# Kernel tuning notes

Hardware: AMD Instinct MI355X
Metric: run time of the kernel (lower is better)

Reference implementation:

```python
import jax, jax.numpy as jnp
from jax import lax
import numpy as np

B, ENC, H, DE, T = 16384, 512, 256, 32, 64


def setup_inputs() -> dict:
    key = jax.random.key(0)
    ks = jax.random.split(key, 12)
    s = lambda fan: 1.0 / np.sqrt(fan)
    return {
        "encoded_input_series": jax.random.normal(ks[0], (B, ENC), jnp.float32),
        "final_x_val": jax.random.normal(ks[1], (B, 1), jnp.float32),
        # embed_func: Dense(DE) applied to scalar input (last dim = 1)
        "W_emb": jax.random.normal(ks[2], (1, DE), jnp.float32) * s(1),
        "b_emb": jnp.zeros((DE,), jnp.float32),
        # encode_reshape layer: Dense(H) on encoded series -> initial h
        "W_enc": jax.random.normal(ks[3], (ENC, H), jnp.float32) * s(ENC),
        "b_enc": jnp.zeros((H,), jnp.float32),
        # LSTM cell params (Keras gate order i, f, c, o)
        "W_k": jax.random.normal(ks[4], (DE, 4 * H), jnp.float32) * s(DE),
        "W_r": jax.random.normal(ks[5], (H, 4 * H), jnp.float32) * s(H),
        "b_lstm": jnp.concatenate([jnp.zeros((H,)), jnp.ones((H,)), jnp.zeros((2 * H,))]).astype(jnp.float32),
        # reduce layer: Dense(1)
        "W_red": jax.random.normal(ks[6], (H, 1), jnp.float32) * s(H),
        "b_red": jnp.zeros((1,), jnp.float32),
        "decode_length": T,
    }


def reference(encoded_input_series, final_x_val, W_emb, b_emb, W_enc, b_enc,
              W_k, W_r, b_lstm, W_red, b_red, decode_length):
    Hdim = W_r.shape[0]
    # initial hidden state from encoder summary; cell state zero-initialized
    h0 = encoded_input_series @ W_enc + b_enc            # [B, H]
    c0 = jnp.zeros_like(h0)
    # initial decoder input: embed of last observed value
    x0 = final_x_val @ W_emb + b_emb                     # [B, DE]

    def step(carry, _):
        h, c, x = carry
        gates = x @ W_k + h @ W_r + b_lstm               # [B, 4H]
        i, f, cb, o = jnp.split(gates, 4, axis=-1)
        c_new = jax.nn.sigmoid(f) * c + jax.nn.sigmoid(i) * jnp.tanh(cb)
        h_new = jax.nn.sigmoid(o) * jnp.tanh(c_new)
        y = h_new @ W_red + b_red                        # [B, 1]
        x_next = y @ W_emb + b_emb
        return (h_new, c_new, x_next), y[:, 0]

    _, ys = lax.scan(step, (h0, c0, x0), None, length=decode_length)
    return ys.T                                          # [B, T]
```

## Files before the change

### kernel.cpp

```cpp
#include <hip/hip_runtime.h>
#include <hip/hip_bf16.h>
#include <math.h>


typedef _Float16 f16x8 __attribute__((ext_vector_type(8)));
typedef float f32x4 __attribute__((ext_vector_type(4)));

#define DEV __device__ __forceinline__

constexpr int ENC = 512;
constexpr int HD  = 256;
constexpr int DE  = 32;
constexpr int TT  = 64;
constexpr int NG  = 4 * HD;
constexpr int NKT = 8;
constexpr int TS  = 528;
constexpr int BR  = 64;
constexpr int NMT = 4;
constexpr int NW  = 16;
constexpr int WRS = 36;

constexpr float L2E = 1.44269504088896f;

DEV bool is_f32(const void* blstm) {
  return ((const unsigned*)blstm)[256] == 0x3F800000u;
}
DEV float ldf(const void* p, size_t i, bool f32) {
  return f32 ? ((const float*)p)[i]
             : __bfloat162float(((const __hip_bfloat16*)p)[i]);
}
DEV float gscale(int n) {
  return ((n >> 8) == 2) ? (2.0f * L2E) : L2E;
}
DEV void split2h(float v, _Float16& hi, _Float16& lo) {
  hi = (_Float16)v;
  lo = (_Float16)(v - (float)hi);
}
DEV void ld8cvt2h(const void* p, size_t i, bool f32, f16x8& hi, f16x8& lo) {
  if (f32) {
    const f32x4* q = (const f32x4*)((const float*)p + i);
    f32x4 u0 = q[0], u1 = q[1];
#pragma unroll
    for (int j = 0; j < 4; ++j) {
      float a = u0[j], b = u1[j];
      _Float16 ah = (_Float16)a, bh = (_Float16)b;
      hi[j] = ah; hi[4 + j] = bh;
      lo[j] = (_Float16)(a - (float)ah); lo[4 + j] = (_Float16)(b - (float)bh);
    }
  } else {
    const __hip_bfloat16* s = (const __hip_bfloat16*)p + i;
#pragma unroll
    for (int j = 0; j < 8; ++j) {
      float a = __bfloat162float(s[j]);
      _Float16 ah = (_Float16)a;
      hi[j] = ah;
      lo[j] = (_Float16)(a - (float)ah);
    }
  }
}
DEV f16x8 load8h(const _Float16* p) {
  return *reinterpret_cast<const f16x8*>(p);
}

DEV void waitflag(volatile int* f, int v) {
  while (*f < v) { __builtin_amdgcn_s_sleep(1); }
  asm volatile("" ::: "memory");
}
DEV void signalflag(volatile int* f, int v, int lane) {
  asm volatile("s_waitcnt lgkmcnt(0)" ::: "memory");
  if (lane == 0) *f = v;
}

__global__ __launch_bounds__(256) void pack_vec(const void* __restrict__ wemb,
                                                const void* __restrict__ bemb,
                                                const void* __restrict__ wk,
                                                const void* __restrict__ bl,
                                                const void* __restrict__ bredp,
                                                float* __restrict__ wk2n,
                                                float* __restrict__ wk2P,
                                                float* __restrict__ bp0P,
                                                float* __restrict__ bp2P) {
  const bool f32 = is_f32(bl);
  int n = blockIdx.x * 256 + threadIdx.x;
  if (n >= NG) return;
  float s1 = 0.f, s2 = 0.f;
  for (int j = 0; j < DE; ++j) {
    float wkv = ldf(wk, (size_t)j * NG + n, f32);
    s1 += ldf(wemb, j, f32) * wkv;
    s2 += ldf(bemb, j, f32) * wkv;
  }
  float b = s2 + ldf(bl, n, f32);
  float sc = gscale(n);
  int g = n >> 8, hcol = n & 255;
  wk2n[n] = s1;
  wk2P[hcol * 4 + g] = s1 * sc;
  bp0P[hcol * 4 + g] = b * sc;
  bp2P[hcol * 4 + g] = (b + ldf(bredp, 0, f32) * s1) * sc;
}

__global__ __launch_bounds__(256) void pack_w(const void* __restrict__ wr,
                                              const void* __restrict__ bl,
                                              const void* __restrict__ wred,
                                              const float* __restrict__ wk2n,
                                              _Float16* __restrict__ d0,
                                              _Float16* __restrict__ d1) {
  const bool f32 = is_f32(bl);
  int idx = blockIdx.x * 256 + threadIdx.x;
  if (idx >= NKT * 64 * 64) return;
  int lane = idx & 63, tile = idx >> 6;
  int nt = tile & 63, ks = tile >> 6;
  int kb = ks * 32 + ((lane >> 4) << 3);
  int n  = (nt << 4) + (lane & 15);
  float wn = wk2n[n];
  float sc = gscale(n);
#pragma unroll
  for (int j = 0; j < 8; ++j) {
    int k = kb + j;
    float v = ldf(wr, (size_t)k * NG + n, f32);
    d0[idx * 8 + j] = (_Float16)(v * sc);
    d1[idx * 8 + j] = (_Float16)((v + ldf(wred, k, f32) * wn) * sc);
  }
}

__global__ __launch_bounds__(256) void pack_e(const void* __restrict__ we,
                                              const void* __restrict__ bl,
                                              _Float16* __restrict__ dhi,
                                              _Float16* __restrict__ dlo) {
  const bool f32 = is_f32(bl);
  int idx = blockIdx.x * 256 + threadIdx.x;
  if (idx >= 16 * 16 * 64) return;
  int lane = idx & 63, tile = idx >> 6;
  int nt = tile & 15, ks = tile >> 4;
  int kb = ks * 32 + ((lane >> 4) << 3);
  int n  = (nt << 4) + (lane & 15);
#pragma unroll
  for (int j = 0; j < 8; ++j) {
    float v = ldf(we, (size_t)(kb + j) * HD + n, f32);
    _Float16 h, l;
    split2h(v, h, l);
    dhi[idx * 8 + j] = h;
    dlo[idx * 8 + j] = l;
  }
}

__global__ __launch_bounds__(1024)
__attribute__((amdgpu_waves_per_eu(4, 4)))
void lstm_main(
    const void* __restrict__ enc,
    const void* __restrict__ fx,
    const void* __restrict__ benc,
    const void* __restrict__ blstm,
    const void* __restrict__ wred,
    const void* __restrict__ bredp,
    const _Float16* __restrict__ pW0,
    const _Float16* __restrict__ pW1,
    const _Float16* __restrict__ pEhi,
    const _Float16* __restrict__ pElo,
    const float* __restrict__ wk2P,
    const float* __restrict__ bp0P,
    const float* __restrict__ bp2P,
    const int* __restrict__ dlen,
    void* __restrict__ out) {
  __shared__ __align__(16) _Float16 frag[2][NMT * NKT * TS];
  __shared__ __align__(16) float bp0L[NG];
  __shared__ __align__(16) float wk2L[NG];
  __shared__ __align__(16) float bp2L[NG];
  __shared__ __align__(16) float wredfP[16 * WRS];
  __shared__ __align__(16) float fxL[BR];
  __shared__ int flagv[NW];

  const bool f32 = is_f32(blstm);
  const int tid  = threadIdx.x;
  const int w    = tid >> 6;
  const int lane = tid & 63;
  const int q    = lane >> 4;
  const int cl   = lane & 15;
  const int r0   = blockIdx.x * BR;
  int Tn = dlen[0];
  if (Tn < 1 || Tn > TT) Tn = TT;

  const int aoff = lane * 8;
  const int hcol = w * 16 + cl;
  const int hwb = (w >> 1) * TS + q * 32 +
                  128 * ((w & 1) * 2 + (cl >> 3)) + (cl & 7);

  const int yrow  = tid >> 4, ypart = tid & 15;
  const int ybase = ((yrow >> 4) * NKT + (ypart >> 1)) * TS +
                    ((yrow & 15) + 16 * ((ypart & 1) * 2)) * 8;
  const int yws   = ypart * WRS;

  if (tid < HD) wredfP[(tid >> 4) * WRS + (tid & 15)] = ldf(wred, tid, f32);
  if (tid < BR) fxL[tid] = ldf(fx, r0 + tid, f32);
  if (tid < NW) flagv[tid] = 0;
  bp0L[tid] = bp0P[tid];
  bp2L[tid] = bp2P[tid];
  wk2L[tid] = wk2P[tid];
  const float bredf = ldf(bredp, 0, f32);

  f32x4 acc0[NMT];
  {
    float be = ldf(benc, hcol, f32);
#pragma unroll
    for (int mt = 0; mt < NMT; ++mt) acc0[mt] = (f32x4){be, be, be, be};
  }
  const size_t ebase = ((size_t)w * 64 + lane) * 8;
#pragma unroll 1
  for (int ks = 0; ks < ENC / 32; ++ks) {
    size_t fo = ebase + (size_t)(ks * 16) * 512;
    f16x8 bh  = load8h(pEhi + fo);
    f16x8 bl2 = load8h(pElo + fo);
#pragma unroll
    for (int mt = 0; mt < NMT; ++mt) {
      f16x8 ah, al;
      ld8cvt2h(enc, (size_t)(r0 + mt * 16 + cl) * ENC + ks * 32 + q * 8, f32, ah, al);
      acc0[mt] = __builtin_amdgcn_mfma_f32_16x16x32_f16(ah, bh,  acc0[mt], 0, 0, 0);
      acc0[mt] = __builtin_amdgcn_mfma_f32_16x16x32_f16(al, bh,  acc0[mt], 0, 0, 0);
      acc0[mt] = __builtin_amdgcn_mfma_f32_16x16x32_f16(ah, bl2, acc0[mt], 0, 0, 0);
    }
  }
#pragma unroll
  for (int mt = 0; mt < NMT; ++mt)
#pragma unroll
    for (int r = 0; r < 4; ++r)
      frag[0][mt * NKT * TS + hwb + r * 8] = (_Float16)acc0[mt][r];

  f32x4 cst[NMT];
#pragma unroll
  for (int mt = 0; mt < NMT; ++mt) cst[mt] = (f32x4){0.f, 0.f, 0.f, 0.f};

  __syncthreads();

  const _Float16* wbase0 = pW0 + ((size_t)w * 64 + lane) * 8;
  const _Float16* wbase1 = pW1 + ((size_t)w * 64 + lane) * 8;

#pragma unroll 1
  for (int t = 0; t < Tn; ++t) {
    const _Float16* FH = &frag[t & 1][0];
    _Float16* WH = &frag[(t + 1) & 1][0];

    f32x4 acc[NMT][4];
    if (t == 0) {
      f32x4 b0 = *(const f32x4*)&bp0L[hcol * 4];
      f32x4 wk = *(const f32x4*)&wk2L[hcol * 4];
#pragma unroll
      for (int mt = 0; mt < NMT; ++mt)
#pragma unroll
        for (int r = 0; r < 4; ++r) {
          float fxr = fxL[mt * 16 + q * 4 + r];
#pragma unroll
          for (int g = 0; g < 4; ++g) acc[mt][g][r] = b0[g] + fxr * wk[g];
        }
    } else {
      f32x4 bb = *(const f32x4*)&bp2L[hcol * 4];
#pragma unroll
      for (int g = 0; g < 4; ++g)
#pragma unroll
        for (int mt = 0; mt < NMT; ++mt)
          acc[mt][g] = (f32x4){bb[g], bb[g], bb[g], bb[g]};
    }

    const _Float16* wb = (t == 0) ? wbase0 : wbase1;
#pragma unroll 1
    for (int j = 0; j < 8; ++j) {
      int ks = (j + (w >> 1)) & 7;
      waitflag(&flagv[2 * ks], t);
      waitflag(&flagv[2 * ks + 1], t);
      f16x8 bc[4];
#pragma unroll
      for (int g = 0; g < 4; ++g)
        bc[g] = load8h(wb + (size_t)(ks * 64 + g * 16) * 512);
#pragma unroll
      for (int mt = 0; mt < NMT; ++mt) {
        f16x8 ah = load8h(&FH[(mt * NKT + ks) * TS + aoff]);
        __builtin_amdgcn_s_setprio(1);
#pragma unroll
        for (int g = 0; g < 4; ++g)
          acc[mt][g] =
              __builtin_amdgcn_mfma_f32_16x16x32_f16(ah, bc[g], acc[mt][g], 0, 0, 0);
        __builtin_amdgcn_s_setprio(0);
      }
    }

    if (t > 0) {
      float sum = 0.f;
#pragma unroll
      for (int jj = 0; jj < 2; ++jj) {
        f16x8 hv = load8h(&FH[ybase + jj * 128]);
        f32x4 wv0 = *(const f32x4*)&wredfP[yws + jj * 8];
        f32x4 wv1 = *(const f32x4*)&wredfP[yws + jj * 8 + 4];
#pragma unroll
        for (int j = 0; j < 4; ++j) {
          sum += (float)hv[j] * wv0[j];
          sum += (float)hv[4 + j] * wv1[j];
        }
      }
      sum += __shfl_xor(sum, 1);
      sum += __shfl_xor(sum, 2);
      sum += __shfl_xor(sum, 4);
      sum += __shfl_xor(sum, 8);
      if (ypart == 0) {
        float y = sum + bredf;
        size_t oi = (size_t)(r0 + yrow) * TT + (t - 1);
        if (f32) ((float*)out)[oi] = y;
        else     ((__hip_bfloat16*)out)[oi] = __float2bfloat16(y);
      }
    }

#pragma unroll
    for (int mt = 0; mt < NMT; ++mt)
#pragma unroll
      for (int r = 0; r < 4; ++r) {
        float gi = acc[mt][0][r];
        float gf = acc[mt][1][r];
        float gc = acc[mt][2][r];
        float go = acc[mt][3][r];
        float P = __builtin_amdgcn_exp2f(-gi);
        float F = __builtin_amdgcn_exp2f(-gf);
        float Q = __builtin_amdgcn_exp2f(-gc);
        float S = __builtin_amdgcn_exp2f(-go);
        float p1 = 1.0f + P, q1 = 1.0f + Q, f1 = 1.0f + F, s1 = 1.0f + S;
        float pq = p1 * q1;
        float num = cst[mt][r] * pq + (1.0f - Q) * f1;
        float cn  = num * __builtin_amdgcn_rcpf(f1 * pq);
        cst[mt][r] = cn;
        float R = __builtin_amdgcn_exp2f(-2.0f * L2E * cn);
        float hn = (1.0f - R) * __builtin_amdgcn_rcpf(s1 * (1.0f + R));
        WH[mt * NKT * TS + hwb + r * 8] = (_Float16)hn;
      }
    signalflag(&flagv[w], t + 1, lane);
  }

#pragma unroll 1
  for (int s = 0; s < NW; ++s) waitflag(&flagv[s], Tn);
  {
    const _Float16* FH = &frag[Tn & 1][0];
    float sum = 0.f;
#pragma unroll
    for (int jj = 0; jj < 2; ++jj) {
      f16x8 hv = load8h(&FH[ybase + jj * 128]);
      f32x4 wv0 = *(const f32x4*)&wredfP[yws + jj * 8];
      f32x4 wv1 = *(const f32x4*)&wredfP[yws + jj * 8 + 4];
#pragma unroll
      for (int j = 0; j < 4; ++j) {
        sum += (float)hv[j] * wv0[j];
        sum += (float)hv[4 + j] * wv1[j];
      }
    }
    sum += __shfl_xor(sum, 1);
    sum += __shfl_xor(sum, 2);
    sum += __shfl_xor(sum, 4);
    sum += __shfl_xor(sum, 8);
    if (ypart == 0) {
      float y = sum + bredf;
      size_t oi = (size_t)(r0 + yrow) * TT + (Tn - 1);
      if (f32) ((float*)out)[oi] = y;
      else     ((__hip_bfloat16*)out)[oi] = __float2bfloat16(y);
    }
  }
}

extern "C" void kernel_launch(void* const* d_in, const int* in_sizes, int n_in,
                              void* d_out, int out_size, void* d_ws, size_t ws_size,
                              hipStream_t stream) {
  const void* enc  = d_in[0];
  const void* fx   = d_in[1];
  const void* wemb = d_in[2];
  const void* bemb = d_in[3];
  const void* wenc = d_in[4];
  const void* benc = d_in[5];
  const void* wk   = d_in[6];
  const void* wr   = d_in[7];
  const void* bl   = d_in[8];
  const void* wred = d_in[9];
  const void* bred = d_in[10];
  const int* dlen  = (const int*)d_in[11];

  _Float16* pW0 = (_Float16*)d_ws;
  _Float16* pW1 = pW0 + NKT * 64 * 64 * 8;
  _Float16* pEhi = pW1 + NKT * 64 * 64 * 8;
  _Float16* pElo = pEhi + 16 * 16 * 64 * 8;
  float* wk2n = (float*)(pElo + 16 * 16 * 64 * 8);
  float* wk2P = wk2n + NG;
  float* bp0P = wk2P + NG;
  float* bp2P = bp0P + NG;

  pack_vec<<<4, 256, 0, stream>>>(wemb, bemb, wk, bl, bred, wk2n, wk2P, bp0P, bp2P);
  pack_w<<<128, 256, 0, stream>>>(wr, bl, wred, wk2n, pW0, pW1);
  pack_e<<<64, 256, 0, stream>>>(wenc, bl, pEhi, pElo);

  int nblocks = in_sizes[1] / BR;
  lstm_main<<<nblocks, 1024, 0, stream>>>(enc, fx, benc, bl, wred, bred,
                                          pW0, pW1, pEhi, pElo, wk2P, bp0P,
                                          bp2P, dlen, d_out);
}
```

Before: 779.9 us.

## Split per-wave LDS flags into half-tile flags to pipeline cell update with consumers

Replaces the single per-wave completion flag with packed 16-bit flags, one per half of the row tiles (mt 0-1 and mt 2-3). Consumers wait on one 32-bit word covering both producer waves and can begin MFMAs on the first half before the second half is written. The wait is moved after the weight loads so global loads overlap the wait. The spin loop drops s_sleep, and the y-reduction reads of the previous h are hoisted ahead of the cell update. The finer-grained signalling adds more LDS flag traffic, and busy spinning without sleep may take issue slots from other waves.

```diff
diff --git a/kernel.cpp b/kernel.cpp
--- a/kernel.cpp
+++ b/kernel.cpp
@@ -62,13 +62,15 @@
   return *reinterpret_cast<const f16x8*>(p);
 }
 
-DEV void waitflag(volatile int* f, int v) {
-  while (*f < v) { __builtin_amdgcn_s_sleep(1); }
+DEV void waitword(volatile short* base, int idx2, int v) {
+  volatile int* p = (volatile int*)(base + idx2);
+  int x = *p;
+  while ((x & 0xffff) < v || ((x >> 16) & 0xffff) < v) { x = *p; }
   asm volatile("" ::: "memory");
 }
-DEV void signalflag(volatile int* f, int v, int lane) {
+DEV void signalhalf(volatile short* base, int w, int half, int v, int lane) {
   asm volatile("s_waitcnt lgkmcnt(0)" ::: "memory");
-  if (lane == 0) *f = v;
+  if (lane == 0) base[(w >> 1) * 4 + 2 * half + (w & 1)] = (short)v;
 }
 
 __global__ __launch_bounds__(256) void pack_vec(const void* __restrict__ wemb,
@@ -167,7 +169,7 @@
   __shared__ __align__(16) float bp2L[NG];
   __shared__ __align__(16) float wredfP[16 * WRS];
   __shared__ __align__(16) float fxL[BR];
-  __shared__ int flagv[NW];
+  __shared__ __align__(4) short flagv[NKT * 4];
 
   const bool f32 = is_f32(blstm);
   const int tid  = threadIdx.x;
@@ -191,7 +193,7 @@
 
   if (tid < HD) wredfP[(tid >> 4) * WRS + (tid & 15)] = ldf(wred, tid, f32);
   if (tid < BR) fxL[tid] = ldf(fx, r0 + tid, f32);
-  if (tid < NW) flagv[tid] = 0;
+  if (tid < NKT * 4) flagv[tid] = 0;
   bp0L[tid] = bp0P[tid];
   bp2L[tid] = bp2P[tid];
   wk2L[tid] = wk2P[tid];
@@ -233,6 +235,29 @@
   const _Float16* wbase0 = pW0 + ((size_t)w * 64 + lane) * 8;
   const _Float16* wbase1 = pW1 + ((size_t)w * 64 + lane) * 8;
 
+#define CELL_MT(MT)                                                        \
+  {                                                                        \
+    _Pragma("unroll")                                                      \
+    for (int r = 0; r < 4; ++r) {                                          \
+      float gi = acc[MT][0][r];                                            \
+      float gf = acc[MT][1][r];                                            \
+      float gc = acc[MT][2][r];                                            \
+      float go = acc[MT][3][r];                                            \
+      float P = __builtin_amdgcn_exp2f(-gi);                               \
+      float F = __builtin_amdgcn_exp2f(-gf);                               \
+      float Q = __builtin_amdgcn_exp2f(-gc);                               \
+      float S = __builtin_amdgcn_exp2f(-go);                               \
+      float p1 = 1.0f + P, q1 = 1.0f + Q, f1 = 1.0f + F, s1 = 1.0f + S;    \
+      float pq = p1 * q1;                                                  \
+      float num = cst[MT][r] * pq + (1.0f - Q) * f1;                       \
+      float cn  = num * __builtin_amdgcn_rcpf(f1 * pq);                    \
+      cst[MT][r] = cn;                                                     \
+      float R = __builtin_amdgcn_exp2f(-2.0f * L2E * cn);                  \
+      float hn = (1.0f - R) * __builtin_amdgcn_rcpf(s1 * (1.0f + R));      \
+      WH[MT * NKT * TS + hwb + r * 8] = (_Float16)hn;                      \
+    }                                                                      \
+  }
+
 #pragma unroll 1
   for (int t = 0; t < Tn; ++t) {
     const _Float16* FH = &frag[t & 1][0];
@@ -263,14 +288,13 @@
 #pragma unroll 1
     for (int j = 0; j < 8; ++j) {
       int ks = (j + (w >> 1)) & 7;
-      waitflag(&flagv[2 * ks], t);
-      waitflag(&flagv[2 * ks + 1], t);
       f16x8 bc[4];
 #pragma unroll
       for (int g = 0; g < 4; ++g)
         bc[g] = load8h(wb + (size_t)(ks * 64 + g * 16) * 512);
-#pragma unroll
-      for (int mt = 0; mt < NMT; ++mt) {
+      waitword(flagv, ks * 4, t);
+#pragma unroll
+      for (int mt = 0; mt < 2; ++mt) {
         f16x8 ah = load8h(&FH[(mt * NKT + ks) * TS + aoff]);
         __builtin_amdgcn_s_setprio(1);
 #pragma unroll
@@ -279,20 +303,41 @@
               __builtin_amdgcn_mfma_f32_16x16x32_f16(ah, bc[g], acc[mt][g], 0, 0, 0);
         __builtin_amdgcn_s_setprio(0);
       }
-    }
+      waitword(flagv, ks * 4 + 2, t);
+#pragma unroll
+      for (int mt = 2; mt < 4; ++mt) {
+        f16x8 ah = load8h(&FH[(mt * NKT + ks) * TS + aoff]);
+        __builtin_amdgcn_s_setprio(1);
+#pragma unroll
+        for (int g = 0; g < 4; ++g)
+          acc[mt][g] =
+              __builtin_amdgcn_mfma_f32_16x16x32_f16(ah, bc[g], acc[mt][g], 0, 0, 0);
+        __builtin_amdgcn_s_setprio(0);
+      }
+    }
+
+    f16x8 hv0 = load8h(&FH[ybase]);
+    f16x8 hv1 = load8h(&FH[ybase + 128]);
+
+    CELL_MT(0)
+    CELL_MT(1)
+    signalhalf(flagv, w, 0, t + 1, lane);
+    CELL_MT(2)
+    CELL_MT(3)
+    signalhalf(flagv, w, 1, t + 1, lane);
 
     if (t > 0) {
+      f32x4 wv00 = *(const f32x4*)&wredfP[yws];
+      f32x4 wv01 = *(const f32x4*)&wredfP[yws + 4];
+      f32x4 wv10 = *(const f32x4*)&wredfP[yws + 8];
+      f32x4 wv11 = *(const f32x4*)&wredfP[yws + 12];
       float sum = 0.f;
 #pragma unroll
-      for (int jj = 0; jj < 2; ++jj) {
-        f16x8 hv = load8h(&FH[ybase + jj * 128]);
-        f32x4 wv0 = *(const f32x4*)&wredfP[yws + jj * 8];
-        f32x4 wv1 = *(const f32x4*)&wredfP[yws + jj * 8 + 4];
-#pragma unroll
-        for (int j = 0; j < 4; ++j) {
-          sum += (float)hv[j] * wv0[j];
-          sum += (float)hv[4 + j] * wv1[j];
-        }
+      for (int j = 0; j < 4; ++j) {
+        sum += (float)hv0[j] * wv00[j];
+        sum += (float)hv0[4 + j] * wv01[j];
+        sum += (float)hv1[j] * wv10[j];
+        sum += (float)hv1[4 + j] * wv11[j];
       }
       sum += __shfl_xor(sum, 1);
       sum += __shfl_xor(sum, 2);
@@ -305,46 +350,28 @@
         else     ((__hip_bfloat16*)out)[oi] = __float2bfloat16(y);
       }
     }
-
-#pragma unroll
-    for (int mt = 0; mt < NMT; ++mt)
-#pragma unroll
-      for (int r = 0; r < 4; ++r) {
-        float gi = acc[mt][0][r];
-        float gf = acc[mt][1][r];
-        float gc = acc[mt][2][r];
-        float go = acc[mt][3][r];
-        float P = __builtin_amdgcn_exp2f(-gi);
-        float F = __builtin_amdgcn_exp2f(-gf);
-        float Q = __builtin_amdgcn_exp2f(-gc);
-        float S = __builtin_amdgcn_exp2f(-go);
-        float p1 = 1.0f + P, q1 = 1.0f + Q, f1 = 1.0f + F, s1 = 1.0f + S;
-        float pq = p1 * q1;
-        float num = cst[mt][r] * pq + (1.0f - Q) * f1;
-        float cn  = num * __builtin_amdgcn_rcpf(f1 * pq);
-        cst[mt][r] = cn;
-        float R = __builtin_amdgcn_exp2f(-2.0f * L2E * cn);
-        float hn = (1.0f - R) * __builtin_amdgcn_rcpf(s1 * (1.0f + R));
-        WH[mt * NKT * TS + hwb + r * 8] = (_Float16)hn;
-      }
-    signalflag(&flagv[w], t + 1, lane);
   }
 
 #pragma unroll 1
-  for (int s = 0; s < NW; ++s) waitflag(&flagv[s], Tn);
+  for (int s = 0; s < NKT; ++s) {
+    waitword(flagv, s * 4, Tn);
+    waitword(flagv, s * 4 + 2, Tn);
+  }
   {
     const _Float16* FH = &frag[Tn & 1][0];
+    f16x8 hv0 = load8h(&FH[ybase]);
+    f16x8 hv1 = load8h(&FH[ybase + 128]);
+    f32x4 wv00 = *(const f32x4*)&wredfP[yws];
+    f32x4 wv01 = *(const f32x4*)&wredfP[yws + 4];
+    f32x4 wv10 = *(const f32x4*)&wredfP[yws + 8];
+    f32x4 wv11 = *(const f32x4*)&wredfP[yws + 12];
     float sum = 0.f;
 #pragma unroll
-    for (int jj = 0; jj < 2; ++jj) {
-      f16x8 hv = load8h(&FH[ybase + jj * 128]);
-      f32x4 wv0 = *(const f32x4*)&wredfP[yws + jj * 8];
-      f32x4 wv1 = *(const f32x4*)&wredfP[yws + jj * 8 + 4];
-#pragma unroll
-      for (int j = 0; j < 4; ++j) {
-        sum += (float)hv[j] * wv0[j];
-        sum += (float)hv[4 + j] * wv1[j];
-      }
+    for (int j = 0; j < 4; ++j) {
+      sum += (float)hv0[j] * wv00[j];
+      sum += (float)hv0[4 + j] * wv01[j];
+      sum += (float)hv1[j] * wv10[j];
+      sum += (float)hv1[4 + j] * wv11[j];
     }
     sum += __shfl_xor(sum, 1);
     sum += __shfl_xor(sum, 2);
@@ -357,6 +384,7 @@
       else     ((__hip_bfloat16*)out)[oi] = __float2bfloat16(y);
     }
   }
+#undef CELL_MT
 }
 
 extern "C" void kernel_launch(void* const* d_in, const int* in_sizes, int n_in,
```

Measured after the change: 799.3 us. +2.5%, slower.
